# Kernel optimization log

Hardware: AMD Instinct MI355X
Metric: run time of the kernel (lower is better)

Reference implementation:

```python
import jax, jax.numpy as jnp
from jax import lax
import numpy as np

EMBED = 256; MDIM = 256; DSTATE = 128; DCONV = 4
NHEADS = 8; HEADDIM = 64; DINNER = 512            # expand=2 -> d_inner=512; headdim 64 -> 8 heads
CONVDIM = DINNER + 2 * DSTATE                      # 768: conv runs over x,B,C channels
DINPROJ = 2 * DINNER + 2 * DSTATE + NHEADS         # 1288
B = 4; H = 64; W = 64; L = H * W

def _ln(x, g, b, eps=1e-5):
    mu = x.mean(-1, keepdims=True)
    v = ((x - mu) ** 2).mean(-1, keepdims=True)
    return (x - mu) / jnp.sqrt(v + eps) * g + b

def _bn(x, g, b, m, v, eps=1e-5):  # x: (B,C,H,W); eval-mode BatchNorm2d
    return (x - m[:, None, None]) / jnp.sqrt(v[:, None, None] + eps) * g[:, None, None] + b[:, None, None]

def _mamba_branch(seq, ln_g, ln_b, in_W, in_b, cw, cb, A_log, Dh, dt_bias, norm_g, out_W, out_b):
    # Pre-LN Mamba2 block with residual. seq: (B, L, MDIM)
    bsz, slen, _ = seq.shape
    x = _ln(seq, ln_g, ln_b)
    zxbcdt = x @ in_W.T + in_b                                   # (B,L,DINPROJ)
    z = zxbcdt[..., :DINNER]
    xBC = zxbcdt[..., DINNER:DINNER + CONVDIM]
    dt = zxbcdt[..., DINNER + CONVDIM:]                          # (B,L,NHEADS)
    # depthwise causal conv1d over sequence dim
    xc = lax.conv_general_dilated(xBC.transpose(0, 2, 1), cw[:, None, :], (1,),
                                  [(DCONV - 1, 0)], feature_group_count=CONVDIM)
    xBC = jax.nn.silu(xc.transpose(0, 2, 1) + cb)
    xh = xBC[..., :DINNER].reshape(bsz, slen, NHEADS, HEADDIM)
    Bm = xBC[..., DINNER:DINNER + DSTATE]                        # (B,L,N)
    Cm = xBC[..., DINNER + DSTATE:]                              # (B,L,N)
    dt = jax.nn.softplus(dt + dt_bias)                           # (B,L,H)
    dA = jnp.exp(dt * (-jnp.exp(A_log)))                         # (B,L,H)
    dtx = dt[..., None] * xh                                     # (B,L,H,P)
    def step(h, inp):
        dA_t, dtx_t, B_t, C_t = inp
        h = h * dA_t[:, :, None, None] + dtx_t[..., None] * B_t[:, None, None, :]
        return h, jnp.einsum('bhpn,bn->bhp', h, C_t)
    h0 = jnp.zeros((bsz, NHEADS, HEADDIM, DSTATE), seq.dtype)
    xs = (dA.transpose(1, 0, 2), dtx.transpose(1, 0, 2, 3),
          Bm.transpose(1, 0, 2), Cm.transpose(1, 0, 2))
    _, ys = lax.scan(step, h0, xs)                               # (L,B,H,P)
    y = ys.transpose(1, 0, 2, 3) + Dh[None, None, :, None] * xh
    y = y.reshape(bsz, slen, DINNER) * jax.nn.silu(z)            # gate
    y = y / jnp.sqrt((y ** 2).mean(-1, keepdims=True) + 1e-5) * norm_g  # RMSNormGated
    return seq + (y @ out_W.T + out_b)

def _forward(curr_bev, prev_bev, conv3_w, bn3_g, bn3_b, bn3_m, bn3_v, conv1_w, bn1_g, bn1_b, bn1_m, bn1_v, fuse_W, fuse_b, ln_g, ln_b, inp_W, inp_b, m_ln_g, m_ln_b, m_in_W, m_in_b, conv_w, conv_b, A_log, Dp, dt_bias, m_norm_g, m_out_W, m_out_b, outp_W, outp_b, bev_h, bev_w):
    b, l, c = curr_bev.shape
    curr = curr_bev.reshape(b, bev_h, bev_w, c)
    prev = prev_bev.reshape(b, bev_h, bev_w, c)  # delta_yaw is None -> no alignment
    cat = jnp.concatenate([curr, prev], -1).transpose(0, 3, 1, 2)         # (B,2C,H,W)
    b3 = _bn(lax.conv_general_dilated(cat, conv3_w, (1, 1), [(1, 1), (1, 1)]), bn3_g, bn3_b, bn3_m, bn3_v)
    b1 = _bn(lax.conv_general_dilated(cat, conv1_w, (1, 1), [(0, 0), (0, 0)]), bn1_g, bn1_b, bn1_m, bn1_v)
    z = jax.nn.relu(jnp.concatenate([b3, b1], 1)).transpose(0, 2, 3, 1)   # (B,H,W,C)
    z = _ln(z @ fuse_W.T + fuse_b, ln_g, ln_b)
    fl = z.reshape(b, l, c)                                               # row-major forward
    fu = z.transpose(0, 2, 1, 3).reshape(b, l, c)                         # column-major forward
    seqs = jnp.stack([fl, fu, fl[:, ::-1], fu[:, ::-1]], 0)               # (4,B,L,C)
    def branch(seq, iW, ib, lg, lb, mW, mb, cw, cb, al, dh, db, ng, oW, ob, pW, pb):
        s = seq @ iW.T + ib
        s = _mamba_branch(s, lg, lb, mW, mb, cw, cb, al, dh, db, ng, oW, ob)
        return s @ pW.T + pb
    outs = jax.vmap(branch)(seqs, inp_W, inp_b, m_ln_g, m_ln_b, m_in_W, m_in_b, conv_w, conv_b, A_log, Dp, dt_bias, m_norm_g, m_out_W, m_out_b, outp_W, outp_b)
    ofl = outs[0].reshape(b, bev_h, bev_w, c)
    ofu = outs[1].reshape(b, bev_w, bev_h, c).transpose(0, 2, 1, 3)
    orl = outs[2][:, ::-1].reshape(b, bev_h, bev_w, c)
    oru = outs[3][:, ::-1].reshape(b, bev_w, bev_h, c).transpose(0, 2, 1, 3)
    fused = 0.25 * (ofl + ofu + orl + oru)
    return curr_bev + fused.reshape(b, l, c)  # resid dropout = identity at inference

def setup_inputs() -> dict:
    key = jax.random.key(0)
    ks = jax.random.split(key, 16)
    rn = lambda k, s, sc=0.02: jax.random.normal(k, s, jnp.float32) * sc
    return {
        "curr_bev": jax.random.normal(ks[0], (B, L, EMBED), jnp.float32),
        "prev_bev": jax.random.normal(ks[1], (B, L, EMBED), jnp.float32),
        "conv3_w": rn(ks[2], (EMBED // 2, 2 * EMBED, 3, 3)),
        "bn3_g": jnp.ones((EMBED // 2,)), "bn3_b": jnp.zeros((EMBED // 2,)),
        "bn3_m": jnp.zeros((EMBED // 2,)), "bn3_v": jnp.ones((EMBED // 2,)),
        "conv1_w": rn(ks[3], (EMBED // 2, 2 * EMBED, 1, 1)),
        "bn1_g": jnp.ones((EMBED // 2,)), "bn1_b": jnp.zeros((EMBED // 2,)),
        "bn1_m": jnp.zeros((EMBED // 2,)), "bn1_v": jnp.ones((EMBED // 2,)),
        "fuse_W": rn(ks[4], (EMBED, EMBED)), "fuse_b": jnp.zeros((EMBED,)),
        "ln_g": jnp.ones((EMBED,)), "ln_b": jnp.zeros((EMBED,)),
        "inp_W": rn(ks[5], (4, MDIM, EMBED)), "inp_b": jnp.zeros((4, MDIM)),
        "m_ln_g": jnp.ones((4, MDIM)), "m_ln_b": jnp.zeros((4, MDIM)),
        "m_in_W": rn(ks[6], (4, DINPROJ, MDIM)), "m_in_b": jnp.zeros((4, DINPROJ)),
        "conv_w": rn(ks[7], (4, CONVDIM, DCONV), 0.1), "conv_b": jnp.zeros((4, CONVDIM)),
        "A_log": jnp.tile(jnp.log(jnp.arange(1, NHEADS + 1, dtype=jnp.float32)), (4, 1)),
        "Dp": jnp.ones((4, NHEADS)),
        "dt_bias": rn(ks[8], (4, NHEADS), 0.1),
        "m_norm_g": jnp.ones((4, DINNER)),
        "m_out_W": rn(ks[9], (4, MDIM, DINNER)), "m_out_b": jnp.zeros((4, MDIM)),
        "outp_W": rn(ks[10], (4, EMBED, MDIM)), "outp_b": jnp.zeros((4, EMBED)),
        "bev_h": H, "bev_w": W,
    }

def reference(curr_bev, prev_bev, conv3_w, bn3_g, bn3_b, bn3_m, bn3_v, conv1_w, bn1_g, bn1_b, bn1_m, bn1_v, fuse_W, fuse_b, ln_g, ln_b, inp_W, inp_b, m_ln_g, m_ln_b, m_in_W, m_in_b, conv_w, conv_b, A_log, Dp, dt_bias, m_norm_g, m_out_W, m_out_b, outp_W, outp_b, bev_h, bev_w):
    return _forward(curr_bev, prev_bev, conv3_w, bn3_g, bn3_b, bn3_m, bn3_v, conv1_w, bn1_g, bn1_b, bn1_m, bn1_v, fuse_W, fuse_b, ln_g, ln_b, inp_W, inp_b, m_ln_g, m_ln_b, m_in_W, m_in_b, conv_w, conv_b, A_log, Dp, dt_bias, m_norm_g, m_out_W, m_out_b, outp_W, outp_b, bev_h, bev_w)
```

## Files before the change

kernel.cpp:

```cpp
#include <hip/hip_runtime.h>
#include <hip/hip_bf16.h>
#include <cstdint>
#include <cstddef>

typedef unsigned short u16;
typedef unsigned int u32;
typedef __attribute__((ext_vector_type(8))) __bf16 bfx8;
typedef __attribute__((ext_vector_type(4))) float f32x4;

static __device__ __forceinline__ float bitf(u32 v){ float f; __builtin_memcpy(&f,&v,4); return f; }
static __device__ __forceinline__ float bf2f(u16 v){ return bitf(((u32)v)<<16); }
static __device__ __forceinline__ u16 f2bf(float f){ __bf16 b=(__bf16)f; u16 r; __builtin_memcpy(&r,&b,2); return r; }
static __device__ __forceinline__ u32 pk2(float a,float b){ return (u32)f2bf(a) | ((u32)f2bf(b)<<16); }
static __device__ __forceinline__ void unpk8(uint4 r, float* o){
  o[0]=bitf(r.x<<16); o[1]=bitf(r.x&0xffff0000u);
  o[2]=bitf(r.y<<16); o[3]=bitf(r.y&0xffff0000u);
  o[4]=bitf(r.z<<16); o[5]=bitf(r.z&0xffff0000u);
  o[6]=bitf(r.w<<16); o[7]=bitf(r.w&0xffff0000u);
}
static __device__ __forceinline__ void unpk4(uint2 r, float* o){
  o[0]=bitf(r.x<<16); o[1]=bitf(r.x&0xffff0000u);
  o[2]=bitf(r.y<<16); o[3]=bitf(r.y&0xffff0000u);
}
static __device__ __forceinline__ void async16(void* lds, const void* g){
// ... 70 lines not shown
      const u16* gb = Bbase + (size_t)(n0+row) * ldb + k0 + ch*8;
      async16(&smB[(size_t)(it*256 + (tid & ~63))*8], gb);
    }
    __syncthreads();
    #pragma unroll
    for (int kk=0; kk<2; ++kk) {
      bfx8 av[4], bv[4];
      #pragma unroll
      for (int mi=0; mi<4; ++mi) {
        int ra = wr*64 + mi*16 + (l & 15);
        av[mi] = *(const bfx8*)&smA[ra*64 + kk*32 + (l>>4)*8];
      }
      #pragma unroll
      for (int ni=0; ni<4; ++ni) {
        int rb = wc*64 + ni*16 + (l & 15);
        bv[ni] = *(const bfx8*)&smB[rb*64 + kk*32 + (l>>4)*8];
      }
      #pragma unroll
      for (int mi=0; mi<4; ++mi)
        #pragma unroll
        for (int ni=0; ni<4; ++ni)
          acc[mi][ni] = __builtin_amdgcn_mfma_f32_16x16x32_bf16(av[mi], bv[ni], acc[mi][ni], 0, 0, 0);
    }
    __syncthreads();
  }

  const float* bias_d = (EPI == 0 || EPI == 3 || EPI == 5) ? g.bias + (size_t)z * g.biasZ : nullptr;
  const u16* add_d = (EPI == 3 || EPI == 5) ? g.add + (size_t)z * g.addZ : nullptr;
  const float* rowsc_d = (EPI == 5) ? g.rowsc + (size_t)z * g.rowscZ : nullptr;
  u16* Cd = g.C + (size_t)z * g.cZ;
  float* Cf = (float*)g.C + (size_t)z * g.cZ;
  #pragma unroll
  for (int mi=0; mi<4; ++mi) {
    #pragma unroll
    for (int ni=0; ni<4; ++ni) {
      f32x4 v = acc[mi][ni];
      const int gr = r0 + wr*64 + mi*16 + ((l >> 4) << 2);
      const int gc = n0 + wc*64 + ni*16 + (l & 15);
      #pragma unroll
      for (int q=0; q<4; ++q) {
        const int r = gr + q;
        float x = v[q];
        if (EPI == 2) {
          x = fmaxf(fmaf(x, g.scale[gc], g.shift[gc]), 0.f);
          Cd[(size_t)r * g.ldc + g.colOff + gc] = f2bf(x);
        } else if (EPI == 3) {
          x += bias_d[gc] + bf2f(add_d[(size_t)r * g.ldc + gc]);
          Cd[(size_t)r * g.ldc + g.colOff + gc] = f2bf(x);
        } else if (EPI == 5) {
          x = x * rowsc_d[r] + bias_d[gc] + bf2f(add_d[(size_t)r * g.ldc + gc]);
          Cd[(size_t)r * g.ldc + g.colOff + gc] = f2bf(x);
        } else if (EPI == 4) {
          Cf[(size_t)r * g.ldc + g.colOff + gc] = x;
        } else {
          x += bias_d[gc];
          Cd[(size_t)r * g.ldc + g.colOff + gc] = f2bf(x);
        }
      }
    }
  }
}

__global__ void castk(const float* __restrict__ s, u16* __restrict__ d, int n)
{
  int i = (blockIdx.x*256 + threadIdx.x)*4;
  if (i < n){
    float4 v = *(const float4*)(s+i);
    ushort4 o; o.x=f2bf(v.x); o.y=f2bf(v.y); o.z=f2bf(v.z); o.w=f2bf(v.w);
    *(ushort4*)(d+i) = o;
  }
}

__global__ void castg(const float* __restrict__ s, const float* __restrict__ gw,
                      u16* __restrict__ d)
{
  int i = (blockIdx.x*256 + threadIdx.x)*4;
  int dd = i >> 17, k = i & 511;
  float4 v = *(const float4*)(s+i);
  float4 g4 = *(const float4*)(gw + dd*512 + k);
  ushort4 o; o.x=f2bf(v.x*g4.x); o.y=f2bf(v.y*g4.y); o.z=f2bf(v.z*g4.z); o.w=f2bf(v.w*g4.w);
  *(ushort4*)(d+i) = o;
}

__global__ void c3rep(const float* __restrict__ w, u16* __restrict__ o)
{
  int id = blockIdx.x*256 + threadIdx.x;
  int oc = id / 4608, rem = id % 4608;
  int tap = rem >> 9, ic = rem & 511;
  o[id] = f2bf(w[((size_t)oc*512 + ic)*9 + tap]);
}

__global__ void bnssk(const float* g3,const float* b3,const float* m3,const float* v3,
                      const float* g1,const float* b1,const float* m1,const float* v1,
                      float* out)
{
  int t = threadIdx.x; int i = t & 127;
  if (t < 128){ float sc = g3[i]*rsqrtf(v3[i]+1e-5f); out[i]=sc; out[128+i]=b3[i]-m3[i]*sc; }
  else        { float sc = g1[i]*rsqrtf(v1[i]+1e-5f); out[256+i]=sc; out[384+i]=b1[i]-m1[i]*sc; }
}

__global__ __launch_bounds__(256)
void c3red(const float* __restrict__ P, const float* __restrict__ bnss, u16* __restrict__ zin)
{
  const int id = blockIdx.x*256 + threadIdx.x;
  const size_t base = (size_t)id * 4;
  const int r = (int)(base >> 7), c = (int)(base & 127);
  float4 s = {0.f,0.f,0.f,0.f};
  #pragma unroll
  for (int z=0; z<9; ++z){
    float4 v = *(const float4*)(P + (size_t)z*2097152 + base);
    s.x += v.x; s.y += v.y; s.z += v.z; s.w += v.w;
  }
  float4 sc = *(const float4*)(bnss + c);
  float4 sh = *(const float4*)(bnss + 128 + c);
  ushort4 o;
  o.x = f2bf(fmaxf(fmaf(s.x, sc.x, sh.x), 0.f));
  o.y = f2bf(fmaxf(fmaf(s.y, sc.y, sh.y), 0.f));
  o.z = f2bf(fmaxf(fmaf(s.z, sc.z, sh.z), 0.f));
  o.w = f2bf(fmaxf(fmaf(s.w, sc.w, sh.w), 0.f));
  *(ushort4*)(zin + (size_t)r*256 + c) = o;
}

__global__ __launch_bounds__(256)
void padk(const float* __restrict__ curr, const float* __restrict__ prev, u16* __restrict__ pad)
{
  const int id = blockIdx.x*256 + threadIdx.x;
  const int c8 = id & 63;
  int t = id >> 6;
  const int xx = t % 66; t /= 66;
  const int yy = t % 66; const int b = t / 66;
  const int c0 = c8*8;
  uint4 o;
  if (yy==0 || yy==65 || xx==0 || xx==65){ o.x=0;o.y=0;o.z=0;o.w=0; }
  else {
    const int l = (yy-1)*64 + (xx-1);
    const float* s = (c0 < 256) ? curr + ((size_t)b*4096 + l)*256 + c0
                                : prev + ((size_t)b*4096 + l)*256 + (c0-256);
    float4 a = *(const float4*)s, bb = *(const float4*)(s+4);
    o.x = pk2(a.x,a.y); o.y = pk2(a.z,a.w); o.z = pk2(bb.x,bb.y); o.w = pk2(bb.z,bb.w);
  }
  *(uint4*)(pad + (((size_t)b*66 + yy)*66 + xx)*512 + c0) = o;
}

__global__ __launch_bounds__(256)
void ln256(const u16* __restrict__ in, long inZ, u16* __restrict__ out, long outZ,
           const float* __restrict__ gw, const float* __restrict__ bw, int pz)
{
  const int z = blockIdx.z;
  const int row = blockIdx.x*4 + (threadIdx.x>>6);
  const int l = threadIdx.x & 63;
  const u16* ip = in + (size_t)z*inZ + (size_t)row*256 + l*4;
  ushort4 rr = *(const ushort4*)ip;
  float v0=bf2f(rr.x), v1=bf2f(rr.y), v2=bf2f(rr.z), v3=bf2f(rr.w);
  float s = v0+v1+v2+v3;
  float ss = v0*v0+v1*v1+v2*v2+v3*v3;
  #pragma unroll
  for(int m=1;m<64;m<<=1){ s += __shfl_xor(s,m); ss += __shfl_xor(ss,m); }
  float mu = s*(1.f/256.f);
  float var = ss*(1.f/256.f) - mu*mu;
  float rs = rsqrtf(var + 1e-5f);
  const float* g = gw + (size_t)z*pz; const float* b = bw + (size_t)z*pz;
  int c = l*4;
  u16* op = out + (size_t)z*outZ + (size_t)row*256 + c;
  ushort4 o; o.x=f2bf((v0-mu)*rs*g[c]+b[c]); o.y=f2bf((v1-mu)*rs*g[c+1]+b[c+1]);
  o.z=f2bf((v2-mu)*rs*g[c+2]+b[c+2]); o.w=f2bf((v3-mu)*rs*g[c+3]+b[c+3]);
  *(ushort4*)op = o;
}

__global__ __launch_bounds__(256)
void rnormk(const u16* __restrict__ Y, float* __restrict__ RS)
{
  const int z = blockIdx.z;
  const int row = blockIdx.x*4 + (threadIdx.x>>6);
  const int l = threadIdx.x & 63;
  const u16* p = Y + ((size_t)z*16384 + row)*512 + l*8;
  uint4 raw = *(const uint4*)p;
  float v[8]; unpk8(raw, v);
  float ss = 0.f;
  #pragma unroll
  for (int j=0;j<8;j++) ss += v[j]*v[j];
  #pragma unroll
  for (int m=1;m<64;m<<=1) ss += __shfl_xor(ss, m);
  if (l == 0) RS[(size_t)z*16384 + row] = rsqrtf(ss*(1.f/512.f) + 1e-5f);
}

__global__ __launch_bounds__(256)
void dtk(const u16* __restrict__ xln, const float* __restrict__ minW,
         const float* __restrict__ minB, const float* __restrict__ dtb,
         float* __restrict__ DT)
{
  __shared__ float sx[32*257];
  const int z = blockIdx.z;
  const int r0 = blockIdx.x * 32;
  const int tid = threadIdx.x;
  {
    const int rr = tid >> 3, cc = (tid & 7) * 32;
    const u16* src = xln + ((size_t)z*16384 + r0 + rr)*256 + cc;
    #pragma unroll
    for (int q=0;q<4;q++){
      uint4 raw = *(const uint4*)(src + q*8);
      float v[8]; unpk8(raw, v);
      #pragma unroll
      for (int j=0;j<8;j++) sx[rr*257 + cc + q*8 + j] = v[j];
    }
  }
  __syncthreads();
  const int ri = tid >> 3, hv = tid & 7;
  const float* wrow = minW + ((size_t)z*1288 + 1280 + hv)*256;
  float acc = 0.f;
  #pragma unroll 4
  for (int k=0; k<256; k+=4){
    float4 wq = *(const float4*)(wrow + k);
    acc += sx[ri*257+k]*wq.x + sx[ri*257+k+1]*wq.y + sx[ri*257+k+2]*wq.z + sx[ri*257+k+3]*wq.w;
  }
  acc += minB[(size_t)z*1288 + 1280 + hv] + dtb[z*8 + hv];
  float dt = (acc > 20.f) ? acc : log1pf(expf(acc));
  DT[((size_t)z*16384 + r0 + ri)*8 + hv] = dt;
}

__global__ __launch_bounds__(256)
void cak(const float* __restrict__ DT, float* __restrict__ CA,
         const float* __restrict__ alog, int dirBase)
{
  const int z = blockIdx.z;
  const int gidx = blockIdx.x*4 + (threadIdx.x>>6);
  const int lane = threadIdx.x & 63;
  const int c = gidx & 63, bh = gidx >> 6;
  const int b = bh >> 3, hh = bh & 7;
  const size_t row = (size_t)z*16384 + (size_t)b*4096 + c*64 + lane;
  float x = DT[row*8 + hh];
  #pragma unroll
  for (int m=1;m<64;m<<=1){ float o = __shfl_up(x, m); if (lane >= m) x += o; }
  float eA = expf(alog[(dirBase+z)*8 + hh]);
  CA[row*8 + hh] = -eA * x;
}

__global__ __launch_bounds__(256)
void convbc(const u16* __restrict__ xbcr, u16* __restrict__ bcc,
            const float* __restrict__ cw, const float* __restrict__ cb)
{
  __shared__ float cwS[4][256];
  __shared__ float cbS[256];
  const int tid = threadIdx.x;
  const int id = blockIdx.x*256 + tid;
  const int c8 = id & 31;
  const int r = (id >> 5) & 16383;
  const int d = id >> 19;
  {
    float4 w4 = *(const float4*)(cw + ((size_t)d*768 + 512 + tid)*4);
    cwS[0][tid]=w4.x; cwS[1][tid]=w4.y; cwS[2][tid]=w4.z; cwS[3][tid]=w4.w;
    cbS[tid] = cb[(size_t)d*768 + 512 + tid];
  }
  __syncthreads();
  const int li = r & 4095;
  const int col = 512 + c8*8;
  const u16* base = xbcr + (size_t)d*16777216 + (size_t)(r - li)*768 + col;
  float acc[8];
  #pragma unroll
  for (int j=0;j<8;j++) acc[j] = cbS[c8*8+j];
  #pragma unroll
  for (int tap=0; tap<4; ++tap){
    int lt = li - 3 + tap;
    if (lt >= 0){
      uint4 raw = *(const uint4*)(base + (size_t)lt*768);
      float v[8]; unpk8(raw, v);
      #pragma unroll
      for (int j=0;j<8;j++)
        acc[j] = fmaf(v[j], cwS[tap][c8*8+j], acc[j]);
    }
  }
  uint4 o;
  float s[8];
  #pragma unroll
  for (int j=0;j<8;j++) s[j] = acc[j] / (1.f + __expf(-acc[j]));
  o.x = pk2(s[0],s[1]); o.y = pk2(s[2],s[3]); o.z = pk2(s[4],s[5]); o.w = pk2(s[6],s[7]);
  *(uint4*)(bcc + ((size_t)d*16384 + r)*256 + c8*8) = o;
}

__global__ __launch_bounds__(256)
void convx(const u16* __restrict__ xbcr, u16* __restrict__ xct,
           const float* __restrict__ cw, const float* __restrict__ cb)
{
  __shared__ u16 T[128*72];
  __shared__ float cwX[4][128];
  __shared__ float cbX[128];
  const int bx = blockIdx.x, z = blockIdx.z;
  const int pq = bx & 3, c = (bx>>2) & 63, b = bx >> 8;
  const int tid = threadIdx.x;
  const u16* xb = xbcr + (size_t)z*16777216 + (size_t)b*4096*768;
  if (tid < 128){
    float4 w4 = *(const float4*)(cw + (size_t)z*3072 + (pq*128+tid)*4);
    cwX[0][tid]=w4.x; cwX[1][tid]=w4.y; cwX[2][tid]=w4.z; cwX[3][tid]=w4.w;
    cbX[tid] = cb[z*768 + pq*128 + tid];
  }
  __syncthreads();
  #pragma unroll
  for (int u=0; u<4; ++u){
    int idx = u*256 + tid;
    int s = idx >> 4, seg = idx & 15;
    int li = c*64 + s;
    int col = pq*128 + seg*8;
    float acc[8];
    #pragma unroll
    for (int j=0;j<8;j++) acc[j] = cbX[seg*8+j];
    #pragma unroll
    for (int tap=0; tap<4; ++tap){
      int lt = li - 3 + tap;
      if (lt >= 0){
        uint4 raw = *(const uint4*)(xb + (size_t)lt*768 + col);
        float v[8]; unpk8(raw, v);
        #pragma unroll
        for (int j=0;j<8;j++) acc[j] = fmaf(v[j], cwX[tap][seg*8+j], acc[j]);
      }
    }
    #pragma unroll
    for (int j=0;j<8;j++)
      T[(seg*8+j)*72 + s] = f2bf(acc[j] / (1.f + __expf(-acc[j])));
  }
  __syncthreads();
  #pragma unroll
  for (int u=0; u<4; ++u){
    int idx = u*256 + tid;
    int pl = idx >> 3, sg = idx & 7;
    uint4 v = *(const uint4*)&T[pl*72 + sg*8];
    *(uint4*)(xct + (size_t)z*8388608 + (size_t)(pq*128+pl)*16384 + b*4096 + c*64 + sg*8) = v;
  }
}

__global__ __launch_bounds__(256)
void btk(const u16* __restrict__ bcc, u16* __restrict__ bt)
{
  __shared__ u16 T[128*72];
  const int bx = blockIdx.x, z = blockIdx.z;
  const int c = bx & 63, b = bx >> 6;
  const int tid = threadIdx.x;
  const u16* src = bcc + ((size_t)z*16384 + (size_t)b*4096 + c*64)*256;
  #pragma unroll
  for (int u=0; u<4; ++u){
    int idx = u*256 + tid;
    int s = idx >> 4, seg = idx & 15;
    uint4 raw = *(const uint4*)(src + (size_t)s*256 + seg*8);
    u16 t8[8]; *(uint4*)t8 = raw;
    #pragma unroll
    for (int j=0;j<8;j++) T[(seg*8+j)*72 + s] = t8[j];
  }
  __syncthreads();
  #pragma unroll
  for (int u=0; u<4; ++u){
    int idx = u*256 + tid;
    int n = idx >> 3, sg = idx & 7;
    uint4 v = *(const uint4*)&T[n*72 + sg*8];
    *(uint4*)(bt + (size_t)z*2097152 + (size_t)n*16384 + b*4096 + c*64 + sg*8) = v;
  }
}

__global__ __launch_bounds__(256)
void sk(const u16* __restrict__ bcc, u16* __restrict__ SR)
{
  __shared__ u16 Bs[64*136];
  const int bx = blockIdx.x, z = blockIdx.z;
  const int c = bx & 63, b = bx >> 6;
  const int tid = threadIdx.x, l = tid & 63, w = tid >> 6;
  const u16* bcp = bcc + ((size_t)z*16384 + (size_t)b*4096 + c*64)*256;
  bfx8 av[4];
  #pragma unroll
  for (int kk=0; kk<4; ++kk)
    av[kk] = *(const bfx8*)(bcp + (size_t)(w*16 + (l&15))*256 + 128 + kk*32 + (l>>4)*8);
  #pragma unroll
  for (int u=0; u<4; ++u){
    int idx = u*256 + tid; int s = idx >> 4, sg = idx & 15;
    *(uint4*)&Bs[s*136 + sg*8] = *(const uint4*)(bcp + (size_t)s*256 + sg*8);
  }
  __syncthreads();
  f32x4 sacc[4];
  #pragma unroll
  for (int i=0;i<4;i++) sacc[i] = (f32x4){0.f,0.f,0.f,0.f};
  #pragma unroll
  for (int kk=0; kk<4; ++kk)
    #pragma unroll
    for (int st=0; st<4; ++st){
      bfx8 bv = *(const bfx8*)&Bs[(st*16 + (l&15))*136 + kk*32 + (l>>4)*8];
      sacc[st] = __builtin_amdgcn_mfma_f32_16x16x32_bf16(av[kk], bv, sacc[st], 0, 0, 0);
    }
  u16* Sd = SR + ((size_t)z*4 + b)*524288 + (size_t)c*4096;
  const int t0 = w*16 + ((l>>4)<<2);
  #pragma unroll
  for (int st=0; st<4; ++st){
    int s = st*16 + (l&15);
    u32* cp = (u32*)&Sd[(size_t)s*64 + t0];
    cp[0] = pk2(sacc[st][0], sacc[st][1]);
    cp[1] = pk2(sacc[st][2], sacc[st][3]);
  }
}

__global__ __launch_bounds__(256)
void csk(const u16* __restrict__ xct, const u16* __restrict__ bt,
         const float* __restrict__ DT, const float* __restrict__ CA,
         u16* __restrict__ CS)
{
  __shared__ u16 Xw[128*72];
  __shared__ u16 Bt[128*72];
  __shared__ float wS[64*2];
  const int bx = blockIdx.x, z = blockIdx.z;
  const int pq = bx & 3, c = (bx>>2) & 63, b = bx >> 8;
  const int tid = threadIdx.x, l = tid & 63, w = tid >> 6;
  const size_t rowb = (size_t)z*16384 + (size_t)b*4096;
  const int p0 = pq*128;
  if (tid < 128){
    int s = tid & 63, hi = tid >> 6;
    int hh = pq*2 + hi;
    float ca63 = CA[(rowb + c*64 + 63)*8 + hh];
    float cav  = CA[(rowb + c*64 + s)*8 + hh];
    float dtv  = DT[(rowb + c*64 + s)*8 + hh];
    wS[s*2+hi] = __expf(ca63 - cav) * dtv;
  }
  __syncthreads();
  #pragma unroll
  for (int u=0; u<4; ++u){
    int idx = u*256 + tid;
    int pl = idx >> 3, sg = idx & 7;
    int hi = pl >> 6;
    uint4 raw = *(const uint4*)(xct + (size_t)z*8388608 + (size_t)(p0+pl)*16384 + b*4096 + c*64 + sg*8);
    float v[8]; unpk8(raw, v);
    uint4 o;
    o.x = pk2(v[0]*wS[(sg*8+0)*2+hi], v[1]*wS[(sg*8+1)*2+hi]);
    o.y = pk2(v[2]*wS[(sg*8+2)*2+hi], v[3]*wS[(sg*8+3)*2+hi]);
    o.z = pk2(v[4]*wS[(sg*8+4)*2+hi], v[5]*wS[(sg*8+5)*2+hi]);
    o.w = pk2(v[6]*wS[(sg*8+6)*2+hi], v[7]*wS[(sg*8+7)*2+hi]);
    *(uint4*)&Xw[pl*72 + sg*8] = o;
  }
  #pragma unroll
  for (int u=0; u<4; ++u){
    int idx = u*256 + tid;
    int n = idx >> 3, sg = idx & 7;
    *(uint4*)&Bt[n*72 + sg*8] =
      *(const uint4*)(bt + (size_t)z*2097152 + (size_t)n*16384 + b*4096 + c*64 + sg*8);
  }
  __syncthreads();
  f32x4 acc[8][2];
  #pragma unroll
  for (int i=0;i<8;i++)
    #pragma unroll
    for (int j=0;j<2;j++) acc[i][j] = (f32x4){0.f,0.f,0.f,0.f};
  #pragma unroll
// ... 13 lines not shown
  #pragma unroll
  for (int mi=0; mi<8; ++mi){
    #pragma unroll
    for (int ni=0; ni<2; ++ni){
      int gp = p0 + w*32 + ni*16 + (l&15);
      int bhx = b*8 + (gp>>6); int pin = gp & 63;
      int n0 = mi*16 + ((l>>4)<<2);
      u32* cp = (u32*)&CS[(size_t)z*16777216 + (size_t)bhx*524288 + (size_t)c*8192 + (size_t)pin*128 + n0];
      cp[0] = pk2(acc[mi][ni][0], acc[mi][ni][1]);
      cp[1] = pk2(acc[mi][ni][2], acc[mi][ni][3]);
    }
  }
}

__global__ __launch_bounds__(256)
void combk(const u16* __restrict__ CS, const float* __restrict__ CA,
           u16* __restrict__ H)
{
  __shared__ float aL[64];
  const int bx = blockIdx.x;
  const int z = blockIdx.z;
  const int nh = bx & 1, pg = (bx >> 1) & 3, bh = bx >> 3;
  const int b = bh >> 3, hh = bh & 7;
  const int tid = threadIdx.x;
  const int p = pg*16 + (tid >> 4), n = nh*64 + (tid & 15)*4;
  const size_t rowb = (size_t)z*16384 + (size_t)b*4096;
  if (tid < 64) aL[tid] = __expf(CA[(rowb + tid*64 + 63)*8 + hh]);
  __syncthreads();
  const u16* Cs = CS + (size_t)z*16777216 + (size_t)bh*524288 + (size_t)p*128 + n;
  u16* Hd = H + (size_t)z*16777216 + (size_t)bh*524288 + (size_t)p*128 + n;
  float h[4];
  #pragma unroll
  for (int j=0;j<4;j++) h[j]=0.f;
  uint2 pf = *(const uint2*)Cs;
  #pragma unroll 1
  for (int c=0; c<64; ++c){
    uint2 cur = pf;
    if (c < 63) pf = *(const uint2*)(Cs + (size_t)(c+1)*8192);
    uint2 o;
    o.x = pk2(h[0],h[1]); o.y = pk2(h[2],h[3]);
    *(uint2*)(Hd + (size_t)c*8192) = o;
    float v[4]; unpk4(cur, v);
    const float a = aL[c];
    #pragma unroll
    for (int j=0;j<4;j++) h[j] = fmaf(h[j], a, v[j]);
  }
}

__global__ __launch_bounds__(256)
void yk2(const u16* __restrict__ bcc, const u16* __restrict__ xct,
         const u16* __restrict__ SR,
         const float* __restrict__ DT, const float* __restrict__ CA,
         const u16* __restrict__ H, const float* __restrict__ Dp,
         u16* __restrict__ Y)
{
  __shared__ u16 Ss[64*72];
  __shared__ u16 Hs[64*136];
  __shared__ u16 Xt[64*72];
  __shared__ u16 Sm[64*72];
  __shared__ float caL[64], dtL[64];
  const int bx = blockIdx.x, z = blockIdx.z;
  const int c = bx & 63, bh = bx >> 6;
  const int b = bh >> 3, hh = bh & 7;
  const int tid = threadIdx.x, l = tid & 63, w = tid >> 6;
  const size_t rowb = (size_t)z*16384 + (size_t)b*4096;
  const u16* bcp = bcc + (rowb + c*64)*256;
  const u16* Hd = H + (size_t)z*16777216 + (size_t)bh*524288 + (size_t)c*8192;
  const u16* xcp = xct + (size_t)z*8388608 + (size_t)(hh*64)*16384 + b*4096 + c*64;
  const u16* Sd = SR + ((size_t)z*4 + b)*524288 + (size_t)c*4096;
  const float Dh = Dp[z*8 + hh];

  bfx8 av[4];
  #pragma unroll
  for (int kk=0; kk<4; ++kk)
    av[kk] = *(const bfx8*)(bcp + (size_t)(w*16 + (l&15))*256 + 128 + kk*32 + (l>>4)*8);

  if (tid < 64){
    caL[tid] = CA[(rowb + c*64 + tid)*8 + hh];
    dtL[tid] = DT[(rowb + c*64 + tid)*8 + hh];
  }
  #pragma unroll
  for (int u=0; u<2; ++u){
    int idx = u*256 + tid; int s = idx >> 3, sg = idx & 7;
    *(uint4*)&Ss[s*72 + sg*8] = *(const uint4*)(Sd + (size_t)s*64 + sg*8);
  }
  #pragma unroll
  for (int u=0; u<4; ++u){
    int idx = u*256 + tid; int p = idx >> 4, sg = idx & 15;
    *(uint4*)&Hs[p*136 + sg*8] = *(const uint4*)(Hd + (size_t)p*128 + sg*8);
  }
  #pragma unroll
  for (int u=0; u<2; ++u){
    int idx = u*256 + tid; int p = idx >> 3, sg = idx & 7;
    *(uint4*)&Xt[p*72 + sg*8] = *(const uint4*)(xcp + (size_t)p*16384 + sg*8);
  }
  __syncthreads();

  f32x4 acc2[4];
  #pragma unroll
  for (int i=0;i<4;i++) acc2[i] = (f32x4){0.f,0.f,0.f,0.f};
  #pragma unroll
  for (int kk=0; kk<4; ++kk)
    #pragma unroll
    for (int st=0; st<4; ++st){
      bfx8 hv = *(const bfx8*)&Hs[(st*16 + (l&15))*136 + kk*32 + (l>>4)*8];
      acc2[st] = __builtin_amdgcn_mfma_f32_16x16x32_bf16(av[kk], hv, acc2[st], 0, 0, 0);
    }
  #pragma unroll
  for (int st=0; st<4; ++st){
    #pragma unroll
    for (int q=0;q<4;q++){
      int t = w*16 + (l>>4)*4 + q;
      int s = st*16 + (l&15);
      float m = (s <= t) ? __expf(caL[t]-caL[s]) * dtL[s] : 0.f;
      Sm[t*72 + s] = f2bf(bf2f(Ss[s*72 + t]) * m);
    }
  }
  #pragma unroll
  for (int pt=0; pt<4; ++pt)
    #pragma unroll
    for (int q=0;q<4;q++){
      int t = w*16 + (l>>4)*4 + q;
      acc2[pt][q] *= __expf(caL[t]);
    }
  __syncthreads();
  #pragma unroll
  for (int kk=0; kk<2; ++kk){
    bfx8 sv = *(const bfx8*)&Sm[(w*16 + (l&15))*72 + kk*32 + (l>>4)*8];
    #pragma unroll
    for (int pt=0; pt<4; ++pt){
      bfx8 bv = *(const bfx8*)&Xt[(pt*16 + (l&15))*72 + kk*32 + (l>>4)*8];
      acc2[pt] = __builtin_amdgcn_mfma_f32_16x16x32_bf16(sv, bv, acc2[pt], 0, 0, 0);
    }
  }
  u16* Yrow = Y + (rowb + c*64)*512 + hh*64;
  #pragma unroll
  for (int pt=0; pt<4; ++pt){
    #pragma unroll
    for (int q=0;q<4;q++){
      int t = w*16 + (l>>4)*4 + q;
      int p = pt*16 + (l&15);
      float xv = bf2f(Xt[p*72 + t]);
      float zf = bf2f(Yrow[(size_t)t*512 + p]);
      float yv = (acc2[pt][q] + Dh*xv) * (zf/(1.f+__expf(-zf)));
      Yrow[(size_t)t*512 + p] = f2bf(yv);
    }
  }
}

__global__ __launch_bounds__(256)
void finalk(const float* __restrict__ curr, const u16* __restrict__ outs, float* __restrict__ o)
{
  const int row = blockIdx.x*4 + (threadIdx.x>>6);
  const int c4 = (threadIdx.x & 63)*4;
  const int b = row >> 12, li = row & 4095;
  const int T = ((li & 63) << 6) | (li >> 6);
  const size_t rb = (size_t)b*4096;
  const ushort4 a0 = *(const ushort4*)(outs + (size_t)0*4194304 + ((rb+li)*256 + c4));
  const ushort4 a1 = *(const ushort4*)(outs + (size_t)1*4194304 + ((rb+T)*256 + c4));
  const ushort4 a2 = *(const ushort4*)(outs + (size_t)2*4194304 + ((rb+4095-li)*256 + c4));
  const ushort4 a3 = *(const ushort4*)(outs + (size_t)3*4194304 + ((rb+4095-T)*256 + c4));
  float4 cv = *(const float4*)(curr + (size_t)row*256 + c4);
  float4 r;
  r.x = cv.x + 0.25f*(bf2f(a0.x)+bf2f(a1.x)+bf2f(a2.x)+bf2f(a3.x));
  r.y = cv.y + 0.25f*(bf2f(a0.y)+bf2f(a1.y)+bf2f(a2.y)+bf2f(a3.y));
  r.z = cv.z + 0.25f*(bf2f(a0.z)+bf2f(a1.z)+bf2f(a2.z)+bf2f(a3.z));
  r.w = cv.w + 0.25f*(bf2f(a0.w)+bf2f(a1.w)+bf2f(a2.w)+bf2f(a3.w));
  *(float4*)(o + (size_t)row*256 + c4) = r;
}

extern "C" void kernel_launch(void* const* d_in, const int* in_sizes, int n_in,
                              void* d_out, int out_size, void* d_ws, size_t ws_size,
                              hipStream_t stream)
{
  (void)in_sizes; (void)n_in; (void)out_size;
  const float* curr   = (const float*)d_in[0];
  const float* prev   = (const float*)d_in[1];
  const float* conv3w = (const float*)d_in[2];
  const float* bn3g=(const float*)d_in[3], *bn3b=(const float*)d_in[4], *bn3m=(const float*)d_in[5], *bn3v=(const float*)d_in[6];
  const float* conv1w = (const float*)d_in[7];
  const float* bn1g=(const float*)d_in[8], *bn1b=(const float*)d_in[9], *bn1m=(const float*)d_in[10], *bn1v=(const float*)d_in[11];
  const float* fuseW=(const float*)d_in[12], *fuseB=(const float*)d_in[13];
  const float* lng=(const float*)d_in[14], *lnb=(const float*)d_in[15];
  const float* inpW=(const float*)d_in[16], *inpB=(const float*)d_in[17];
  const float* mlng=(const float*)d_in[18], *mlnb=(const float*)d_in[19];
  const float* minW=(const float*)d_in[20], *minB=(const float*)d_in[21];
  const float* cw=(const float*)d_in[22], *cb=(const float*)d_in[23];
  const float* alog=(const float*)d_in[24], *Dp=(const float*)d_in[25], *dtb=(const float*)d_in[26];
  const float* mng=(const float*)d_in[27];
  const float* moutW=(const float*)d_in[28], *moutB=(const float*)d_in[29];
  const float* outpW=(const float*)d_in[30], *outpB=(const float*)d_in[31];

  char* ws = (char*)d_ws;
  size_t off = 0;
  auto alloc = [&](size_t bytes){ size_t o = off; off = (off + bytes + 1023) & ~(size_t)1023; return o; };
  const size_t O_WFUSE = alloc((size_t)256*256*2);
  const size_t O_WINP  = alloc((size_t)4*256*256*2);
  const size_t O_WMIN  = alloc((size_t)4*1288*256*2);
  const size_t O_WMOUT = alloc((size_t)4*256*512*2);
  const size_t O_WOUTP = alloc((size_t)4*256*256*2);
  const size_t O_WC3   = alloc((size_t)128*4608*2);
  const size_t O_WC1   = alloc((size_t)128*512*2);
  const size_t O_BNSS  = alloc(512*4);
  const size_t O_ZF    = alloc((size_t)16384*256*2);
  const size_t O_OUTS  = alloc((size_t)4*16384*256*2);
  const size_t O_P     = off;

  const size_t S0d  = (size_t)16384*256*2;
  const size_t XLNd = (size_t)16384*256*2;
  const size_t Yd   = (size_t)16384*512*2;
  const size_t XCTd = (size_t)512*16384*2;
  const size_t BTd  = (size_t)128*16384*2;
  const size_t DTd  = (size_t)16384*8*4;
  const size_t CAd  = (size_t)16384*8*4;
  const size_t SRd  = (size_t)4*64*4096*2;
  const size_t RSd  = (size_t)16384*4;
  const size_t XHd  = (size_t)16777216*2;
  const size_t perdir = S0d + XLNd + Yd + XCTd + BTd + DTd + CAd + SRd + RSd + XHd;

  const size_t PADsz = (size_t)4*66*66*512*2;
  const size_t CPsz  = (size_t)9*16384*128*4;
  const size_t PREsz = PADsz + CPsz + (size_t)16384*256*2*2 + 4096;

  int nd = 0;
  for (int cand = 4; cand >= 1; cand >>= 1) {
    size_t need = (size_t)cand*perdir; if (need < PREsz) need = PREsz;
    if (O_P + need <= ws_size) { nd = cand; break; }
  }
  if (nd == 0) return;

  #define WP(o) ((u16*)(ws + (o)))
  #define FP(o) ((float*)(ws + (o)))

  const size_t O_PAD = O_P;
  const size_t O_CP  = O_PAD + PADsz;
  const size_t O_ZIN = O_CP + CPsz;
  const size_t O_ZFT = O_ZIN + (size_t)16384*256*2;

  bnssk<<<1, 256, 0, stream>>>(bn3g,bn3b,bn3m,bn3v, bn1g,bn1b,bn1m,bn1v, FP(O_BNSS));
  castk<<<64, 256, 0, stream>>>(fuseW, WP(O_WFUSE), 65536);
  castk<<<256, 256, 0, stream>>>(inpW, WP(O_WINP), 262144);
  castk<<<1288, 256, 0, stream>>>(minW, WP(O_WMIN), 1318912);
  castg<<<512, 256, 0, stream>>>(moutW, mng, WP(O_WMOUT));
  castk<<<256, 256, 0, stream>>>(outpW, WP(O_WOUTP), 262144);
  castk<<<64, 256, 0, stream>>>(conv1w, WP(O_WC1), 65536);
  c3rep<<<2304, 256, 0, stream>>>(conv3w, WP(O_WC3));
  padk<<<4356, 256, 0, stream>>>(curr, prev, WP(O_PAD));

  GemmArgs a;
  a = {}; a.A = WP(O_PAD); a.pad = WP(O_PAD);
  a.Bw = WP(O_WC3); a.bZ = 512; a.ldb = 4608;
  a.C = WP(O_CP); a.cZ = 2097152; a.ldc = 128; a.colOff = 0; a.K = 512;
  gemm_bt<2,4><<<dim3(128,1,9), 256, 0, stream>>>(a);
  c3red<<<2048, 256, 0, stream>>>(FP(O_CP), FP(O_BNSS), WP(O_ZIN));
  a = {}; a.A = WP(O_PAD); a.pad = WP(O_PAD); a.Bw = WP(O_WC1); a.bZ = 0; a.ldb = 512;
  a.scale = FP(O_BNSS)+256; a.shift = FP(O_BNSS)+384;
  a.C = WP(O_ZIN); a.cZ = 0; a.ldc = 256; a.colOff = 128; a.K = 512;
  gemm_bt<3,2><<<dim3(128,1,1), 256, 0, stream>>>(a);
  a = {}; a.A = WP(O_ZIN); a.aZ = 0; a.lda = 256; a.Bw = WP(O_WFUSE); a.bZ = 0; a.ldb = 256;
  a.bias = fuseB; a.biasZ = 0; a.C = WP(O_ZFT); a.cZ = 0; a.ldc = 256; a.colOff = 0; a.K = 256;
  gemm_bt<0,0><<<dim3(128,2,1), 256, 0, stream>>>(a);
  ln256<<<dim3(4096,1,1), 256, 0, stream>>>(WP(O_ZFT), 0, WP(O_ZF), 0, lng, lnb, 0);

  for (int d0 = 0; d0 < 4; d0 += nd) {
    size_t o = O_P;
    const size_t O_S0  = o; o += (size_t)nd*S0d;
    const size_t O_XLN = o; o += (size_t)nd*XLNd;
    const size_t O_Y   = o; o += (size_t)nd*Yd;
    const size_t O_XCT = o; o += (size_t)nd*XCTd;
    const size_t O_BT  = o; o += (size_t)nd*BTd;
    const size_t O_DT  = o; o += (size_t)nd*DTd;
    const size_t O_CA  = o; o += (size_t)nd*CAd;
    const size_t O_SR  = o; o += (size_t)nd*SRd;
    const size_t O_RS  = o; o += (size_t)nd*RSd;
    const size_t O_XH  = o;
    const size_t O_BCC = O_XLN;
    const size_t O_S1  = O_XLN;

    a = {}; a.A = WP(O_ZF); a.aZ = 0; a.lda = 256;
    a.Bw = WP(O_WINP) + (size_t)d0*65536; a.bZ = 65536; a.ldb = 256;
    a.bias = inpB + d0*256; a.biasZ = 256;
    a.C = WP(O_S0); a.cZ = 4194304; a.ldc = 256; a.colOff = 0; a.K = 256; a.dirBase = d0;
    gemm_bt<1,0><<<dim3(128,2,nd), 256, 0, stream>>>(a);
    ln256<<<dim3(4096,1,nd), 256, 0, stream>>>(WP(O_S0), 4194304, WP(O_XLN), 4194304,
                                               mlng + d0*256, mlnb + d0*256, 256);
    dtk<<<dim3(512,1,nd), 256, 0, stream>>>(WP(O_XLN), minW + (size_t)d0*329728,
                                            minB + d0*1288, dtb + d0*8, FP(O_DT));
    cak<<<dim3(512,1,nd), 256, 0, stream>>>(FP(O_DT), FP(O_CA), alog, d0);
    a = {}; a.A = WP(O_XLN); a.aZ = 4194304; a.lda = 256;
    a.Bw = WP(O_WMIN) + (size_t)d0*329728; a.bZ = 329728; a.ldb = 256;
    a.bias = minB + d0*1288; a.biasZ = 1288;
    a.C = WP(O_Y); a.cZ = 8388608; a.ldc = 512; a.colOff = 0; a.K = 256;
    gemm_bt<0,0><<<dim3(128,4,nd), 256, 0, stream>>>(a);
    a = {}; a.A = WP(O_XLN); a.aZ = 4194304; a.lda = 256;
    a.Bw = WP(O_WMIN) + (size_t)d0*329728 + (size_t)512*256; a.bZ = 329728; a.ldb = 256;
    a.bias = minB + d0*1288 + 512; a.biasZ = 1288;
    a.C = WP(O_XH); a.cZ = 16777216; a.ldc = 768; a.colOff = 0; a.K = 256;
    gemm_bt<0,0><<<dim3(128,6,nd), 256, 0, stream>>>(a);
    convbc<<<nd*2048, 256, 0, stream>>>(WP(O_XH), WP(O_BCC), cw + d0*3072, cb + d0*768);
    convx<<<dim3(1024,1,nd), 256, 0, stream>>>(WP(O_XH), WP(O_XCT), cw + d0*3072, cb + d0*768);
    btk<<<dim3(256,1,nd), 256, 0, stream>>>(WP(O_BCC), WP(O_BT));
    sk<<<dim3(256,1,nd), 256, 0, stream>>>(WP(O_BCC), WP(O_SR));
    csk<<<dim3(1024,1,nd), 256, 0, stream>>>(WP(O_XCT), WP(O_BT), FP(O_DT), FP(O_CA), WP(O_XH));
    combk<<<dim3(256,1,nd), 256, 0, stream>>>(WP(O_XH), FP(O_CA), WP(O_XH));
    yk2<<<dim3(2048,1,nd), 256, 0, stream>>>(WP(O_BCC), WP(O_XCT), WP(O_SR),
                                             FP(O_DT), FP(O_CA), WP(O_XH), Dp + d0*8, WP(O_Y));
    rnormk<<<dim3(4096,1,nd), 256, 0, stream>>>(WP(O_Y), FP(O_RS));
    a = {}; a.A = WP(O_Y); a.aZ = 8388608; a.lda = 512;
    a.Bw = WP(O_WMOUT) + (size_t)d0*131072; a.bZ = 131072; a.ldb = 512;
    a.bias = moutB + d0*256; a.biasZ = 256;
    a.add = WP(O_S0); a.addZ = 4194304;
    a.rowsc = FP(O_RS); a.rowscZ = 16384;
    a.C = WP(O_S1); a.cZ = 4194304; a.ldc = 256; a.colOff = 0; a.K = 512;
    gemm_bt<0,5><<<dim3(128,2,nd), 256, 0, stream>>>(a);
    a = {}; a.A = WP(O_S1); a.aZ = 4194304; a.lda = 256;
    a.Bw = WP(O_WOUTP) + (size_t)d0*65536; a.bZ = 65536; a.ldb = 256;
    a.bias = outpB + d0*256; a.biasZ = 256;
    a.C = WP(O_OUTS) + (size_t)d0*4194304; a.cZ = 4194304; a.ldc = 256; a.colOff = 0; a.K = 256;
    gemm_bt<0,0><<<dim3(128,2,nd), 256, 0, stream>>>(a);
  }

  finalk<<<4096, 256, 0, stream>>>(curr, WP(O_OUTS), (float*)d_out);

  #undef WP
  #undef FP
}
```

Baseline: 729.4 us.

## Fuse B/C conv, transpose and S-matrix kernels; fold RMS sum into yk2

Merges convbc, btk and sk into a single bck kernel. It computes the causal conv plus SiLU for the B/C channels into shared memory, writes the transposed B and the C·B chunk matrix from there, and shrinks the SR buffer stride. Replaces the rnormk pass over Y with per-head sum-of-squares partials written by yk2, reduced by a small rsumk kernel. The conv3 partial products are now stored as bf16 rather than fp32, halving c3red traffic at some cost in precision of the 9-way partial sum.

```diff
diff --git a/kernel.cpp b/kernel.cpp
--- a/kernel.cpp
+++ b/kernel.cpp
@@ -146,6 +146,8 @@
           Cd[(size_t)r * g.ldc + g.colOff + gc] = f2bf(x);
         } else if (EPI == 4) {
           Cf[(size_t)r * g.ldc + g.colOff + gc] = x;
+        } else if (EPI == 6) {
+          Cd[(size_t)r * g.ldc + g.colOff + gc] = f2bf(x);
         } else {
           x += bias_d[gc];
           Cd[(size_t)r * g.ldc + g.colOff + gc] = f2bf(x);
@@ -194,25 +196,27 @@
 }
 
 __global__ __launch_bounds__(256)
-void c3red(const float* __restrict__ P, const float* __restrict__ bnss, u16* __restrict__ zin)
+void c3red(const u16* __restrict__ P, const float* __restrict__ bnss, u16* __restrict__ zin)
 {
   const int id = blockIdx.x*256 + threadIdx.x;
-  const size_t base = (size_t)id * 4;
+  const size_t base = (size_t)id * 8;
   const int r = (int)(base >> 7), c = (int)(base & 127);
-  float4 s = {0.f,0.f,0.f,0.f};
+  float s[8] = {0,0,0,0,0,0,0,0};
   #pragma unroll
   for (int z=0; z<9; ++z){
-    float4 v = *(const float4*)(P + (size_t)z*2097152 + base);
-    s.x += v.x; s.y += v.y; s.z += v.z; s.w += v.w;
-  }
-  float4 sc = *(const float4*)(bnss + c);
-  float4 sh = *(const float4*)(bnss + 128 + c);
-  ushort4 o;
-  o.x = f2bf(fmaxf(fmaf(s.x, sc.x, sh.x), 0.f));
-  o.y = f2bf(fmaxf(fmaf(s.y, sc.y, sh.y), 0.f));
-  o.z = f2bf(fmaxf(fmaf(s.z, sc.z, sh.z), 0.f));
-  o.w = f2bf(fmaxf(fmaf(s.w, sc.w, sh.w), 0.f));
-  *(ushort4*)(zin + (size_t)r*256 + c) = o;
+    uint4 raw = *(const uint4*)(P + (size_t)z*2097152 + base);
+    float v[8]; unpk8(raw, v);
+    #pragma unroll
+    for (int j=0;j<8;j++) s[j] += v[j];
+  }
+  uint4 o;
+  float r8[8];
+  #pragma unroll
+  for (int j=0;j<8;j++)
+    r8[j] = fmaxf(fmaf(s[j], bnss[c+j], bnss[128+c+j]), 0.f);
+  o.x = pk2(r8[0],r8[1]); o.y = pk2(r8[2],r8[3]);
+  o.z = pk2(r8[4],r8[5]); o.w = pk2(r8[6],r8[7]);
+  *(uint4*)(zin + (size_t)r*256 + c) = o;
 }
 
 __global__ __launch_bounds__(256)
@@ -262,20 +266,14 @@
 }
 
 __global__ __launch_bounds__(256)
-void rnormk(const u16* __restrict__ Y, float* __restrict__ RS)
+void rsumk(const float* __restrict__ RS8, float* __restrict__ RS)
 {
   const int z = blockIdx.z;
-  const int row = blockIdx.x*4 + (threadIdx.x>>6);
-  const int l = threadIdx.x & 63;
-  const u16* p = Y + ((size_t)z*16384 + row)*512 + l*8;
-  uint4 raw = *(const uint4*)p;
-  float v[8]; unpk8(raw, v);
-  float ss = 0.f;
-  #pragma unroll
-  for (int j=0;j<8;j++) ss += v[j]*v[j];
-  #pragma unroll
-  for (int m=1;m<64;m<<=1) ss += __shfl_xor(ss, m);
-  if (l == 0) RS[(size_t)z*16384 + row] = rsqrtf(ss*(1.f/512.f) + 1e-5f);
+  const int row = blockIdx.x*256 + threadIdx.x;
+  const float* p = RS8 + ((size_t)z*16384 + row)*8;
+  float4 a = *(const float4*)p, b = *(const float4*)(p+4);
+  float s = a.x+a.y+a.z+a.w+b.x+b.y+b.z+b.w;
+  RS[(size_t)z*16384 + row] = rsqrtf(s*(1.f/512.f) + 1e-5f);
 }
 
 __global__ __launch_bounds__(256)
@@ -330,45 +328,86 @@
 }
 
 __global__ __launch_bounds__(256)
-void convbc(const u16* __restrict__ xbcr, u16* __restrict__ bcc,
-            const float* __restrict__ cw, const float* __restrict__ cb)
-{
+void bck(const u16* __restrict__ xbcr, u16* __restrict__ bcc, u16* __restrict__ bt,
+         u16* __restrict__ SR, const float* __restrict__ cw, const float* __restrict__ cb)
+{
+  __shared__ u16 BCs[64*264];
+  __shared__ u16 Tb[128*72];
   __shared__ float cwS[4][256];
   __shared__ float cbS[256];
-  const int tid = threadIdx.x;
-  const int id = blockIdx.x*256 + tid;
-  const int c8 = id & 31;
-  const int r = (id >> 5) & 16383;
-  const int d = id >> 19;
+  const int bx = blockIdx.x, z = blockIdx.z;
+  const int c = bx & 63, b = bx >> 6;
+  const int tid = threadIdx.x, l = tid & 63, w = tid >> 6;
+  const u16* xb = xbcr + (size_t)z*16777216 + (size_t)b*4096*768;
+  const float* cwp = cw + (size_t)z*3072;
+  const float* cbp = cb + (size_t)z*768;
   {
-    float4 w4 = *(const float4*)(cw + ((size_t)d*768 + 512 + tid)*4);
+    float4 w4 = *(const float4*)(cwp + (512 + tid)*4);
     cwS[0][tid]=w4.x; cwS[1][tid]=w4.y; cwS[2][tid]=w4.z; cwS[3][tid]=w4.w;
-    cbS[tid] = cb[(size_t)d*768 + 512 + tid];
-  }
-  __syncthreads();
-  const int li = r & 4095;
-  const int col = 512 + c8*8;
-  const u16* base = xbcr + (size_t)d*16777216 + (size_t)(r - li)*768 + col;
-  float acc[8];
-  #pragma unroll
-  for (int j=0;j<8;j++) acc[j] = cbS[c8*8+j];
-  #pragma unroll
-  for (int tap=0; tap<4; ++tap){
-    int lt = li - 3 + tap;
-    if (lt >= 0){
-      uint4 raw = *(const uint4*)(base + (size_t)lt*768);
-      float v[8]; unpk8(raw, v);
+    cbS[tid] = cbp[512 + tid];
+  }
+  __syncthreads();
+  #pragma unroll
+  for (int u=0; u<8; ++u){
+    int idx = u*256 + tid;
+    int s = idx >> 5, c8 = idx & 31;
+    int li = c*64 + s;
+    int col = 512 + c8*8;
+    float acc[8];
+    #pragma unroll
+    for (int j=0;j<8;j++) acc[j] = cbS[c8*8+j];
+    #pragma unroll
+    for (int tap=0; tap<4; ++tap){
+      int lt = li - 3 + tap;
+      if (lt >= 0){
+        uint4 raw = *(const uint4*)(xb + (size_t)lt*768 + col);
+        float v[8]; unpk8(raw, v);
+        #pragma unroll
+        for (int j=0;j<8;j++) acc[j] = fmaf(v[j], cwS[tap][c8*8+j], acc[j]);
+      }
+    }
+    u16 o8[8];
+    #pragma unroll
+    for (int j=0;j<8;j++) o8[j] = f2bf(acc[j] / (1.f + __expf(-acc[j])));
+    *(uint4*)&BCs[s*264 + c8*8] = *(const uint4*)o8;
+    if (c8 >= 16){
+      *(uint4*)(bcc + ((size_t)z*16384 + (size_t)b*4096 + li)*256 + c8*8) = *(const uint4*)o8;
+    } else {
       #pragma unroll
-      for (int j=0;j<8;j++)
-        acc[j] = fmaf(v[j], cwS[tap][c8*8+j], acc[j]);
-    }
-  }
-  uint4 o;
-  float s[8];
-  #pragma unroll
-  for (int j=0;j<8;j++) s[j] = acc[j] / (1.f + __expf(-acc[j]));
-  o.x = pk2(s[0],s[1]); o.y = pk2(s[2],s[3]); o.z = pk2(s[4],s[5]); o.w = pk2(s[6],s[7]);
-  *(uint4*)(bcc + ((size_t)d*16384 + r)*256 + c8*8) = o;
+      for (int j=0;j<8;j++) Tb[(c8*8+j)*72 + s] = o8[j];
+    }
+  }
+  __syncthreads();
+  bfx8 av[4];
+  #pragma unroll
+  for (int kk=0; kk<4; ++kk)
+    av[kk] = *(const bfx8*)&BCs[(w*16 + (l&15))*264 + 128 + kk*32 + (l>>4)*8];
+  f32x4 sacc[4];
+  #pragma unroll
+  for (int i=0;i<4;i++) sacc[i] = (f32x4){0.f,0.f,0.f,0.f};
+  #pragma unroll
+  for (int kk=0; kk<4; ++kk)
+    #pragma unroll
+    for (int st=0; st<4; ++st){
+      bfx8 bv = *(const bfx8*)&BCs[(st*16 + (l&15))*264 + kk*32 + (l>>4)*8];
+      sacc[st] = __builtin_amdgcn_mfma_f32_16x16x32_bf16(av[kk], bv, sacc[st], 0, 0, 0);
+    }
+  u16* Sd = SR + ((size_t)z*4 + b)*262144 + (size_t)c*4096;
+  const int t0 = w*16 + ((l>>4)<<2);
+  #pragma unroll
+  for (int st=0; st<4; ++st){
+    int s = st*16 + (l&15);
+    u32* cp = (u32*)&Sd[(size_t)s*64 + t0];
+    cp[0] = pk2(sacc[st][0], sacc[st][1]);
+    cp[1] = pk2(sacc[st][2], sacc[st][3]);
+  }
+  #pragma unroll
+  for (int u=0; u<4; ++u){
+    int idx = u*256 + tid;
+    int n = idx >> 3, sg = idx & 7;
+    uint4 v = *(const uint4*)&Tb[n*72 + sg*8];
+    *(uint4*)(bt + (size_t)z*2097152 + (size_t)n*16384 + (size_t)b*4096 + c*64 + sg*8) = v;
+  }
 }
 
 __global__ __launch_bounds__(256)
@@ -418,72 +457,6 @@
     int pl = idx >> 3, sg = idx & 7;
     uint4 v = *(const uint4*)&T[pl*72 + sg*8];
     *(uint4*)(xct + (size_t)z*8388608 + (size_t)(pq*128+pl)*16384 + b*4096 + c*64 + sg*8) = v;
-  }
-}
-
-__global__ __launch_bounds__(256)
-void btk(const u16* __restrict__ bcc, u16* __restrict__ bt)
-{
-  __shared__ u16 T[128*72];
-  const int bx = blockIdx.x, z = blockIdx.z;
-  const int c = bx & 63, b = bx >> 6;
-  const int tid = threadIdx.x;
-  const u16* src = bcc + ((size_t)z*16384 + (size_t)b*4096 + c*64)*256;
-  #pragma unroll
-  for (int u=0; u<4; ++u){
-    int idx = u*256 + tid;
-    int s = idx >> 4, seg = idx & 15;
-    uint4 raw = *(const uint4*)(src + (size_t)s*256 + seg*8);
-    u16 t8[8]; *(uint4*)t8 = raw;
-    #pragma unroll
-    for (int j=0;j<8;j++) T[(seg*8+j)*72 + s] = t8[j];
-  }
-  __syncthreads();
-  #pragma unroll
-  for (int u=0; u<4; ++u){
-    int idx = u*256 + tid;
-    int n = idx >> 3, sg = idx & 7;
-    uint4 v = *(const uint4*)&T[n*72 + sg*8];
-    *(uint4*)(bt + (size_t)z*2097152 + (size_t)n*16384 + b*4096 + c*64 + sg*8) = v;
-  }
-}
-
-__global__ __launch_bounds__(256)
-void sk(const u16* __restrict__ bcc, u16* __restrict__ SR)
-{
-  __shared__ u16 Bs[64*136];
-  const int bx = blockIdx.x, z = blockIdx.z;
-  const int c = bx & 63, b = bx >> 6;
-  const int tid = threadIdx.x, l = tid & 63, w = tid >> 6;
-  const u16* bcp = bcc + ((size_t)z*16384 + (size_t)b*4096 + c*64)*256;
-  bfx8 av[4];
-  #pragma unroll
-  for (int kk=0; kk<4; ++kk)
-    av[kk] = *(const bfx8*)(bcp + (size_t)(w*16 + (l&15))*256 + 128 + kk*32 + (l>>4)*8);
-  #pragma unroll
-  for (int u=0; u<4; ++u){
-    int idx = u*256 + tid; int s = idx >> 4, sg = idx & 15;
-    *(uint4*)&Bs[s*136 + sg*8] = *(const uint4*)(bcp + (size_t)s*256 + sg*8);
-  }
-  __syncthreads();
-  f32x4 sacc[4];
-  #pragma unroll
-  for (int i=0;i<4;i++) sacc[i] = (f32x4){0.f,0.f,0.f,0.f};
-  #pragma unroll
-  for (int kk=0; kk<4; ++kk)
-    #pragma unroll
-    for (int st=0; st<4; ++st){
-      bfx8 bv = *(const bfx8*)&Bs[(st*16 + (l&15))*136 + kk*32 + (l>>4)*8];
-      sacc[st] = __builtin_amdgcn_mfma_f32_16x16x32_bf16(av[kk], bv, sacc[st], 0, 0, 0);
-    }
-  u16* Sd = SR + ((size_t)z*4 + b)*524288 + (size_t)c*4096;
-  const int t0 = w*16 + ((l>>4)<<2);
-  #pragma unroll
-  for (int st=0; st<4; ++st){
-    int s = st*16 + (l&15);
-    u32* cp = (u32*)&Sd[(size_t)s*64 + t0];
-    cp[0] = pk2(sacc[st][0], sacc[st][1]);
-    cp[1] = pk2(sacc[st][2], sacc[st][3]);
   }
 }
 
@@ -603,7 +576,7 @@
          const u16* __restrict__ SR,
          const float* __restrict__ DT, const float* __restrict__ CA,
          const u16* __restrict__ H, const float* __restrict__ Dp,
-         u16* __restrict__ Y)
+         u16* __restrict__ Y, float* __restrict__ RS8)
 {
   __shared__ u16 Ss[64*72];
   __shared__ u16 Hs[64*136];
@@ -618,7 +591,7 @@
   const u16* bcp = bcc + (rowb + c*64)*256;
   const u16* Hd = H + (size_t)z*16777216 + (size_t)bh*524288 + (size_t)c*8192;
   const u16* xcp = xct + (size_t)z*8388608 + (size_t)(hh*64)*16384 + b*4096 + c*64;
-  const u16* Sd = SR + ((size_t)z*4 + b)*524288 + (size_t)c*4096;
+  const u16* Sd = SR + ((size_t)z*4 + b)*262144 + (size_t)c*4096;
   const float Dh = Dp[z*8 + hh];
 
   bfx8 av[4];
@@ -685,6 +658,7 @@
     }
   }
   u16* Yrow = Y + (rowb + c*64)*512 + hh*64;
+  float ssq[4] = {0.f,0.f,0.f,0.f};
   #pragma unroll
   for (int pt=0; pt<4; ++pt){
     #pragma unroll
@@ -694,7 +668,18 @@
       float xv = bf2f(Xt[p*72 + t]);
       float zf = bf2f(Yrow[(size_t)t*512 + p]);
       float yv = (acc2[pt][q] + Dh*xv) * (zf/(1.f+__expf(-zf)));
+      ssq[q] += yv*yv;
       Yrow[(size_t)t*512 + p] = f2bf(yv);
+    }
+  }
+  #pragma unroll
+  for (int q=0;q<4;q++){
+    float s = ssq[q];
+    s += __shfl_xor(s, 1); s += __shfl_xor(s, 2);
+    s += __shfl_xor(s, 4); s += __shfl_xor(s, 8);
+    if ((l & 15) == 0){
+      int t = w*16 + (l>>4)*4 + q;
+      RS8[(rowb + c*64 + t)*8 + hh] = s;
     }
   }
 }
@@ -766,11 +751,12 @@
   const size_t CAd  = (size_t)16384*8*4;
   const size_t SRd  = (size_t)4*64*4096*2;
   const size_t RSd  = (size_t)16384*4;
+  const size_t RS8d = (size_t)16384*8*4;
   const size_t XHd  = (size_t)16777216*2;
-  const size_t perdir = S0d + XLNd + Yd + XCTd + BTd + DTd + CAd + SRd + RSd + XHd;
+  const size_t perdir = S0d + XLNd + Yd + XCTd + BTd + DTd + CAd + SRd + RSd + RS8d + XHd;
 
   const size_t PADsz = (size_t)4*66*66*512*2;
-  const size_t CPsz  = (size_t)9*16384*128*4;
+  const size_t CPsz  = (size_t)9*16384*128*2;
   const size_t PREsz = PADsz + CPsz + (size_t)16384*256*2*2 + 4096;
 
   int nd = 0;
@@ -802,8 +788,8 @@
   a = {}; a.A = WP(O_PAD); a.pad = WP(O_PAD);
   a.Bw = WP(O_WC3); a.bZ = 512; a.ldb = 4608;
   a.C = WP(O_CP); a.cZ = 2097152; a.ldc = 128; a.colOff = 0; a.K = 512;
-  gemm_bt<2,4><<<dim3(128,1,9), 256, 0, stream>>>(a);
-  c3red<<<2048, 256, 0, stream>>>(FP(O_CP), FP(O_BNSS), WP(O_ZIN));
+  gemm_bt<2,6><<<dim3(128,1,9), 256, 0, stream>>>(a);
+  c3red<<<1024, 256, 0, stream>>>(WP(O_CP), FP(O_BNSS), WP(O_ZIN));
   a = {}; a.A = WP(O_PAD); a.pad = WP(O_PAD); a.Bw = WP(O_WC1); a.bZ = 0; a.ldb = 512;
   a.scale = FP(O_BNSS)+256; a.shift = FP(O_BNSS)+384;
   a.C = WP(O_ZIN); a.cZ = 0; a.ldc = 256; a.colOff = 128; a.K = 512;
@@ -824,6 +810,7 @@
     const size_t O_CA  = o; o += (size_t)nd*CAd;
     const size_t O_SR  = o; o += (size_t)nd*SRd;
     const size_t O_RS  = o; o += (size_t)nd*RSd;
+    const size_t O_RS8 = o; o += (size_t)nd*RS8d;
     const size_t O_XH  = o;
     const size_t O_BCC = O_XLN;
     const size_t O_S1  = O_XLN;
@@ -848,15 +835,15 @@
     a.bias = minB + d0*1288 + 512; a.biasZ = 1288;
     a.C = WP(O_XH); a.cZ = 16777216; a.ldc = 768; a.colOff = 0; a.K = 256;
     gemm_bt<0,0><<<dim3(128,6,nd), 256, 0, stream>>>(a);
-    convbc<<<nd*2048, 256, 0, stream>>>(WP(O_XH), WP(O_BCC), cw + d0*3072, cb + d0*768);
     convx<<<dim3(1024,1,nd), 256, 0, stream>>>(WP(O_XH), WP(O_XCT), cw + d0*3072, cb + d0*768);
-    btk<<<dim3(256,1,nd), 256, 0, stream>>>(WP(O_BCC), WP(O_BT));
-    sk<<<dim3(256,1,nd), 256, 0, stream>>>(WP(O_BCC), WP(O_SR));
+    bck<<<dim3(256,1,nd), 256, 0, stream>>>(WP(O_XH), WP(O_BCC), WP(O_BT), WP(O_SR),
+                                            cw + d0*3072, cb + d0*768);
     csk<<<dim3(1024,1,nd), 256, 0, stream>>>(WP(O_XCT), WP(O_BT), FP(O_DT), FP(O_CA), WP(O_XH));
     combk<<<dim3(256,1,nd), 256, 0, stream>>>(WP(O_XH), FP(O_CA), WP(O_XH));
     yk2<<<dim3(2048,1,nd), 256, 0, stream>>>(WP(O_BCC), WP(O_XCT), WP(O_SR),
-                                             FP(O_DT), FP(O_CA), WP(O_XH), Dp + d0*8, WP(O_Y));
-    rnormk<<<dim3(4096,1,nd), 256, 0, stream>>>(WP(O_Y), FP(O_RS));
+                                             FP(O_DT), FP(O_CA), WP(O_XH), Dp + d0*8,
+                                             WP(O_Y), FP(O_RS8));
+    rsumk<<<dim3(64,1,nd), 256, 0, stream>>>(FP(O_RS8), FP(O_RS));
     a = {}; a.A = WP(O_Y); a.aZ = 8388608; a.lda = 512;
     a.Bw = WP(O_WMOUT) + (size_t)d0*131072; a.bZ = 131072; a.ldb = 512;
     a.bias = moutB + d0*256; a.biasZ = 256;
```

Result: faster. 711.7 us (-2.4%).
